# Kernel optimization log

Measured on AMD Instinct MI355X. Metric: run time of the kernel, lower is better.

## Reference

```python
import jax, jax.numpy as jnp
import numpy as np

EMBED_DIM = 1024
PROJ_DIM = 64
B, S = 8, 2048


def setup_inputs() -> dict:
    key = jax.random.key(0)
    k1, k2, k3 = jax.random.split(key, 3)
    context = jax.random.normal(k1, (S, B, EMBED_DIM), dtype=jnp.float32)
    prior = jax.random.uniform(k2, (B, S), dtype=jnp.float32)
    # xavier_uniform for (2*proj_dim, embed_dim)
    bound = float(np.sqrt(6.0 / (2 * PROJ_DIM + EMBED_DIM)))
    proj_weight = jax.random.uniform(k3, (2 * PROJ_DIM, EMBED_DIM), dtype=jnp.float32,
                                     minval=-bound, maxval=bound)
    proj_bias = jnp.zeros((2 * PROJ_DIM,), dtype=jnp.float32)
    return {"context": context, "prior": prior,
            "proj_weight": proj_weight, "proj_bias": proj_bias}


def reference(context, prior, proj_weight, proj_bias):
    # context: (S, B, E) -> (B, S, E)
    x = jnp.transpose(context, (1, 0, 2))
    b, s, e = x.shape
    qk = jnp.einsum('bse,pe->bsp', x, proj_weight) + proj_bias  # (B,S,2P)
    query, key = jnp.split(qk, 2, axis=2)
    # neighbor scores, scaled by embed_dim (as in the original)
    fwd = jnp.sum(query[:, :-1] * key[:, 1:], axis=-1) / e   # (B,S-1) score i<->i+1
    bwd = jnp.sum(query[:, 1:] * key[:, :-1], axis=-1) / e   # (B,S-1) score i<->i-1
    ninf = jnp.full((b, 1), -jnp.inf, dtype=x.dtype)
    score = jnp.stack([jnp.concatenate([fwd, ninf], axis=1),
                       jnp.concatenate([ninf, bwd], axis=1)], axis=-1)  # (B,S,2)
    prob = jax.nn.softmax(score, axis=-1)
    # torch .roll(shifts=-1) with no dims flattens the whole tensor: reproduce that
    shift_prob = jnp.roll(prob[:, :, 1].reshape(-1), -1).reshape(b, s)
    prob0 = jnp.sqrt(prob[:, :, 0] * shift_prob + 1e-6)      # (B,S)
    neighbor_attn = prior + (1.0 - prior) * prob0
    log_prob = jnp.log(neighbor_attn)
    # Original places log_prob[:, :-1] on the superdiagonal and hits it with
    # triu matmuls on both sides: C[i,j] = sum_{m=i}^{j-1} log_prob[m] for j>i.
    # Equivalent O(n^2): prefix sums cs[t] = sum_{m<t} log_prob[m].
    cs = jnp.concatenate([jnp.zeros((b, 1), dtype=x.dtype),
                          jnp.cumsum(log_prob[:, :-1], axis=1)], axis=1)  # (B,S)
    D = cs[:, None, :] - cs[:, :, None]            # D[b,i,j] = cs[j]-cs[i]
    i_idx = jnp.arange(s)
    upper = i_idx[None, :] > i_idx[:, None]        # (S,S) j>i
    M = jnp.where(upper[None], D, -D)              # C + C^T (symmetric)
    constituent_attn = jnp.exp(M)
    diag = i_idx[None, :] == i_idx[:, None]
    constituent_attn = jnp.where(diag[None], jnp.zeros((), x.dtype), constituent_attn)
    return constituent_attn, neighbor_attn
```

## Files before the change

### kernel.cpp

```cpp
#include <hip/hip_runtime.h>
#include <cstdint>
#include <cstddef>

#define E_DIM 1024
#define PD 64
#define NP 128
#define B_DIM 8
#define S_DIM 2048
#define M_TOT (B_DIM * S_DIM)

#define BMR 32
#define BK 32
#define NCHH 16

typedef __attribute__((ext_vector_type(8))) short short8v;
typedef __attribute__((ext_vector_type(4))) float f32x4;

__device__ __forceinline__ void gload16(const void* g, void* l) {
    __builtin_amdgcn_global_load_lds(
        (const __attribute__((address_space(1))) unsigned int*)g,
        (__attribute__((address_space(3))) unsigned int*)(uintptr_t)l,
        16, 0, 0);
}

__device__ __forceinline__ void cvt_hilo(const f32x4 v0, const f32x4 v1,
                                         short8v& h, short8v& l) {
    const unsigned MSK = 0xFFFF0000u;
    unsigned a0 = __float_as_uint(v0.x), a1 = __float_as_uint(v0.y);
    unsigned a2 = __float_as_uint(v0.z), a3 = __float_as_uint(v0.w);
    unsigned a4 = __float_as_uint(v1.x), a5 = __float_as_uint(v1.y);
    unsigned a6 = __float_as_uint(v1.z), a7 = __float_as_uint(v1.w);
    float l0 = v0.x - __uint_as_float(a0 & MSK);
    float l1 = v0.y - __uint_as_float(a1 & MSK);
    float l2 = v0.z - __uint_as_float(a2 & MSK);
    float l3 = v0.w - __uint_as_float(a3 & MSK);
    float l4 = v1.x - __uint_as_float(a4 & MSK);
    float l5 = v1.y - __uint_as_float(a5 & MSK);
    float l6 = v1.z - __uint_as_float(a6 & MSK);
    float l7 = v1.w - __uint_as_float(a7 & MSK);
    union { unsigned u[4]; short8v s; } H, L;
    H.u[0] = (a1 & MSK) | (a0 >> 16);
    H.u[1] = (a3 & MSK) | (a2 >> 16);
    H.u[2] = (a5 & MSK) | (a4 >> 16);
    H.u[3] = (a7 & MSK) | (a6 >> 16);
    L.u[0] = (__float_as_uint(l1) & MSK) | (__float_as_uint(l0) >> 16);
    L.u[1] = (__float_as_uint(l3) & MSK) | (__float_as_uint(l2) >> 16);
    L.u[2] = (__float_as_uint(l5) & MSK) | (__float_as_uint(l4) >> 16);
    L.u[3] = (__float_as_uint(l7) & MSK) | (__float_as_uint(l6) >> 16);
    h = H.s; l = L.s;
}

__global__ __launch_bounds__(256) void conv_w(const float* __restrict__ W,
                                              ushort* __restrict__ hiImg,
                                              ushort* __restrict__ loImg) {
    const int t = blockIdx.x * 256 + threadIdx.x;
    const int c  = t & 127;
    const int q  = (t >> 7) & 3;
    const int ch = t >> 9;
    const float* src = W + (size_t)c * E_DIM + ch * 32 + q * 8;
    const f32x4 v0 = *(const f32x4*)src;
    const f32x4 v1 = *(const f32x4*)(src + 4);
    short8v h, l;
    cvt_hilo(v0, v1, h, l);
    const size_t off = ((size_t)(ch * 4 + q) * NP + c) * 8;
    *(short8v*)&hiImg[off] = h;
    *(short8v*)&loImg[off] = l;
}

__global__ __launch_bounds__(512, 4) void gemm_qk(const float* __restrict__ A,
                                                  const ushort* __restrict__ hiImg,
                                                  const ushort* __restrict__ loImg,
                                                  const float* __restrict__ bias,
                                                  float* __restrict__ qk) {
    __shared__ __align__(16) float As[2][2][BMR][BK];
    __shared__ __align__(16) float Cred[BMR][NP];
    const int tid = threadIdx.x;
    const int m0  = blockIdx.x * BMR;
    const int w   = tid >> 6;
    const int h   = w >> 2;
    const int wv  = w & 3;
    const int ln  = tid & 63;
    const int lr  = ln >> 3;
    const int g8  = ln & 7;
    const int row16 = ln & 15;
    const int kq    = ln >> 4;
    const int r7    = row16 & 7;
    const int sg0 = ((((kq << 1) | 0) ^ r7) & 7) << 2;
    const int sg1 = ((((kq << 1) | 1) ^ r7) & 7) << 2;

    const int srow = wv * 8 + lr;
    const float* aS = A + (size_t)(m0 + srow) * E_DIM + h * (NCHH * BK)
                        + ((g8 ^ (srow & 7)) << 2);
    const ushort* hS = hiImg + (size_t)(h * NCHH) * 4096
                             + ((size_t)kq * NP + wv * 32 + row16) * 8;
    const ushort* lS = loImg + (size_t)(h * NCHH) * 4096
                             + ((size_t)kq * NP + wv * 32 + row16) * 8;

    float bias2[2];
    bias2[0] = bias[wv * 32 + row16];
    bias2[1] = bias[wv * 32 + 16 + row16];

    f32x4 acc[2][2];
#pragma unroll
    for (int i = 0; i < 2; ++i)
#pragma unroll
        for (int j = 0; j < 2; ++j) acc[i][j] = (f32x4){0.f, 0.f, 0.f, 0.f};

    short8v whA0, whA1, wlA0, wlA1;
    short8v whB0, whB1, wlB0, wlB1;

    gload16(aS, &As[h][0][wv * 8][0]);
    whA0 = *(const short8v*)(hS);
    whA1 = *(const short8v*)(hS + 128);
    wlA0 = *(const short8v*)(lS);
    wlA1 = *(const short8v*)(lS + 128);

#define GBODY(CH, WH0, WH1, WL0, WL1, NWH0, NWH1, NWL0, NWL1)                       \
    {                                                                               \
        const int buf = (CH) & 1;                                                   \
        __syncthreads();                    \
        if ((CH) + 1 < NCHH) {                                                      \
            gload16(aS + ((CH) + 1) * BK, &As[h][buf ^ 1][wv * 8][0]);              \
            NWH0 = *(const short8v*)(hS + (size_t)((CH) + 1) * 4096);               \
            NWH1 = *(const short8v*)(hS + (size_t)((CH) + 1) * 4096 + 128);         \
            NWL0 = *(const short8v*)(lS + (size_t)((CH) + 1) * 4096);               \
            NWL1 = *(const short8v*)(lS + (size_t)((CH) + 1) * 4096 + 128);         \
        }                                                                           \
        short8v ah0, al0, ah1, al1;                                                 \
        {                                                                           \
            const float* b0 = &As[h][buf][row16][0];                                \
            cvt_hilo(*(const f32x4*)(b0 + sg0), *(const f32x4*)(b0 + sg1), ah0, al0); \
            const float* b1 = &As[h][buf][16 + row16][0];                           \
            cvt_hilo(*(const f32x4*)(b1 + sg0), *(const f32x4*)(b1 + sg1), ah1, al1); \
        }                                                                           \
        acc[0][0] = __builtin_amdgcn_mfma_f32_16x16x32_bf16(ah0, WH0, acc[0][0], 0, 0, 0); \
        acc[0][0] = __builtin_amdgcn_mfma_f32_16x16x32_bf16(ah0, WL0, acc[0][0], 0, 0, 0); \
        acc[0][0] = __builtin_amdgcn_mfma_f32_16x16x32_bf16(al0, WH0, acc[0][0], 0, 0, 0); \
        acc[0][1] = __builtin_amdgcn_mfma_f32_16x16x32_bf16(ah0, WH1, acc[0][1], 0, 0, 0); \
        acc[0][1] = __builtin_amdgcn_mfma_f32_16x16x32_bf16(ah0, WL1, acc[0][1], 0, 0, 0); \
        acc[0][1] = __builtin_amdgcn_mfma_f32_16x16x32_bf16(al0, WH1, acc[0][1], 0, 0, 0); \
        acc[1][0] = __builtin_amdgcn_mfma_f32_16x16x32_bf16(ah1, WH0, acc[1][0], 0, 0, 0); \
        acc[1][0] = __builtin_amdgcn_mfma_f32_16x16x32_bf16(ah1, WL0, acc[1][0], 0, 0, 0); \
        acc[1][0] = __builtin_amdgcn_mfma_f32_16x16x32_bf16(al1, WH0, acc[1][0], 0, 0, 0); \
        acc[1][1] = __builtin_amdgcn_mfma_f32_16x16x32_bf16(ah1, WH1, acc[1][1], 0, 0, 0); \
        acc[1][1] = __builtin_amdgcn_mfma_f32_16x16x32_bf16(ah1, WL1, acc[1][1], 0, 0, 0); \
        acc[1][1] = __builtin_amdgcn_mfma_f32_16x16x32_bf16(al1, WH1, acc[1][1], 0, 0, 0); \
    }

#pragma unroll 1
    for (int c2 = 0; c2 < NCHH / 2; ++c2) {
        GBODY(2 * c2,     whA0, whA1, wlA0, wlA1, whB0, whB1, wlB0, wlB1)
        GBODY(2 * c2 + 1, whB0, whB1, wlB0, wlB1, whA0, whA1, wlA0, wlA1)
    }
#undef GBODY

    if (h == 1) {
#pragma unroll
        for (int fi = 0; fi < 2; ++fi)
#pragma unroll
            for (int fj = 0; fj < 2; ++fj)
#pragma unroll
                for (int r = 0; r < 4; ++r)
                    Cred[fi * 16 + kq * 4 + r][wv * 32 + fj * 16 + row16] = acc[fi][fj][r];
    }
    __syncthreads();
    if (h == 0) {
#pragma unroll
        for (int fi = 0; fi < 2; ++fi)
#pragma unroll
            for (int fj = 0; fj < 2; ++fj) {
#pragma unroll
                for (int r = 0; r < 4; ++r) {
                    const int mr = fi * 16 + kq * 4 + r;
                    const int p  = wv * 32 + fj * 16 + row16;
                    qk[(size_t)(m0 + mr) * NP + p] =
                        acc[fi][fj][r] + Cred[mr][p] + bias2[fj];
                }
            }
    }
}

__global__ __launch_bounds__(256) void neighbor_probs(const float* __restrict__ qk,
                                                      float* __restrict__ p0,
                                                      float* __restrict__ p1) {
    const int m = blockIdx.x * 4 + (threadIdx.x >> 6);
    const int lane = threadIdx.x & 63;
    const int s = m >> 3;
    const int b = m & 7;

    const float q = qk[(size_t)m * NP + lane];
    const float kn = (s < S_DIM - 1) ? qk[(size_t)(m + B_DIM) * NP + PD + lane] : 0.f;
    const float kp = (s > 0) ? qk[(size_t)(m - B_DIM) * NP + PD + lane] : 0.f;
    float f = q * kn;
    float g = q * kp;
#pragma unroll
    for (int off = 32; off; off >>= 1) {
        f += __shfl_xor(f, off);
        g += __shfl_xor(g, off);
    }
    if (lane == 0) {
        const float s0 = f * (1.f / (float)E_DIM);
        const float s1 = g * (1.f / (float)E_DIM);
        float P0, P1;
        if (s == S_DIM - 1) { P0 = 0.f; P1 = 1.f; }
        else if (s == 0)    { P0 = 1.f; P1 = 0.f; }
        else {
            const float mx = fmaxf(s0, s1);
            const float e0 = __expf(s0 - mx), e1 = __expf(s1 - mx);
            const float inv = 1.f / (e0 + e1);
            P0 = e0 * inv; P1 = e1 * inv;
        }
        p0[b * S_DIM + s] = P0;
        p1[b * S_DIM + s] = P1;
    }
}

__global__ __launch_bounds__(256) void combine_scan(const float* __restrict__ p0,
                                                    const float* __restrict__ p1,
                                                    const float* __restrict__ prior,
                                                    float* __restrict__ out_na,
                                                    float* __restrict__ cs) {
    const int b = blockIdx.x;
    const int tid = threadIdx.x;
    __shared__ float sh[256];

    const int base = b * S_DIM + tid * 8;
    float incl[8];
    float run = 0.f;
#pragma unroll
    for (int u = 0; u < 8; ++u) {
        const int fidx = base + u;
        int nf = fidx + 1;
        if (nf == B_DIM * S_DIM) nf = 0;
        const float P0 = p0[fidx];
        const float sp = p1[nf];
        const float pr = prior[fidx];
        const float na = pr + (1.f - pr) * sqrtf(P0 * sp + 1e-6f);
        out_na[fidx] = na;
        run += __logf(na);
        incl[u] = run;
    }
    sh[tid] = run;
    __syncthreads();
    for (int off = 1; off < 256; off <<= 1) {
        float v = sh[tid];
        if (tid >= off) v += sh[tid - off];
        __syncthreads();
        sh[tid] = v;
        __syncthreads();
    }
    const float offset = (tid > 0) ? sh[tid - 1] : 0.f;
#pragma unroll
    for (int u = 0; u < 8; ++u) {
        cs[base + u] = offset + ((u > 0) ? incl[u - 1] : 0.f);
    }
}

__global__ __launch_bounds__(256) void big_out(const float* __restrict__ cs,
                                               float* __restrict__ out) {
    const int bi = blockIdx.x;
    const int b = bi >> 11;
    const int i = bi & (S_DIM - 1);
    const float ci = cs[b * S_DIM + i];
    const float* crow = cs + (size_t)b * S_DIM;
    float* orow = out + (size_t)bi * S_DIM;
    const int j0 = threadIdx.x * 8;
#pragma unroll
    for (int h = 0; h < 2; ++h) {
        const int j = j0 + h * 4;
        const f32x4 cj = *(const f32x4*)&crow[j];
        f32x4 o;
        {
            const int jj = j + 0; const float m = (jj > i) ? (cj.x - ci) : (ci - cj.x);
            o.x = (jj == i) ? 0.f : __expf(m);
        }
        {
            const int jj = j + 1; const float m = (jj > i) ? (cj.y - ci) : (ci - cj.y);
            o.y = (jj == i) ? 0.f : __expf(m);
        }
        {
            const int jj = j + 2; const float m = (jj > i) ? (cj.z - ci) : (ci - cj.z);
            o.z = (jj == i) ? 0.f : __expf(m);
        }
        {
            const int jj = j + 3; const float m = (jj > i) ? (cj.w - ci) : (ci - cj.w);
            o.w = (jj == i) ? 0.f : __expf(m);
        }
        *(f32x4*)&orow[j] = o;
    }
}

extern "C" void kernel_launch(void* const* d_in, const int* in_sizes, int n_in,
                              void* d_out, int out_size, void* d_ws, size_t ws_size,
                              hipStream_t stream) {
    const float* context = (const float*)d_in[0];
    const float* prior   = (const float*)d_in[1];
    const float* W       = (const float*)d_in[2];
    const float* bias    = (const float*)d_in[3];
    float* out = (float*)d_out;

    float* qk = (float*)d_ws;
    float* p0 = qk + (size_t)M_TOT * NP;
    float* p1 = p0 + M_TOT;
    float* cs = p1 + M_TOT;
    ushort* hiImg = (ushort*)out;
    ushort* loImg = hiImg + (size_t)NP * E_DIM;
    float* na_out = out + (size_t)B_DIM * S_DIM * S_DIM;

    conv_w<<<64, 256, 0, stream>>>(W, hiImg, loImg);
    gemm_qk<<<M_TOT / BMR, 512, 0, stream>>>(context, hiImg, loImg, bias, qk);
    neighbor_probs<<<M_TOT / 4, 256, 0, stream>>>(qk, p0, p1);
    combine_scan<<<B_DIM, 256, 0, stream>>>(p0, p1, prior, na_out, cs);
    big_out<<<M_TOT, 256, 0, stream>>>(cs, out);
}
```

Baseline: 64.04 us.

## Fuse neighbor-score softmax into the projection GEMM with halo rows

The QK projection GEMM now computes the neighbor dot products and the 2-way softmax in its epilogue. It drops the intermediate qk buffer and the separate neighbor_probs kernel. Each block loads 48 context rows, its 32 rows plus an 8-row halo on each side, so neighbor keys are available in shared memory. The split-K across two wave halves is replaced by 4 waves that each walk the full K. This redundantly recomputes the halo rows, adding 50% more GEMM work, and gives fewer waves per block in exchange for removing a global round trip and a launch.

```diff
diff --git a/kernel.cpp b/kernel.cpp
--- a/kernel.cpp
+++ b/kernel.cpp
@@ -9,9 +9,8 @@
 #define S_DIM 2048
 #define M_TOT (B_DIM * S_DIM)
 
-#define BMR 32
 #define BK 32
-#define NCHH 16
+#define NCH (E_DIM / BK)
 
 typedef __attribute__((ext_vector_type(8))) short short8v;
 typedef __attribute__((ext_vector_type(4))) float f32x4;
@@ -50,6 +49,8 @@
     h = H.s; l = L.s;
 }
 
+#define MFMA(d, a, b) d = __builtin_amdgcn_mfma_f32_16x16x32_bf16(a, b, d, 0, 0, 0)
+
 __global__ __launch_bounds__(256) void conv_w(const float* __restrict__ W,
                                               ushort* __restrict__ hiImg,
                                               ushort* __restrict__ loImg) {
@@ -67,18 +68,18 @@
     *(short8v*)&loImg[off] = l;
 }
 
-__global__ __launch_bounds__(512, 4) void gemm_qk(const float* __restrict__ A,
-                                                  const ushort* __restrict__ hiImg,
-                                                  const ushort* __restrict__ loImg,
-                                                  const float* __restrict__ bias,
-                                                  float* __restrict__ qk) {
-    __shared__ __align__(16) float As[2][2][BMR][BK];
-    __shared__ __align__(16) float Cred[BMR][NP];
+__global__ __launch_bounds__(256, 2) void gemm_scores(const float* __restrict__ A,
+                                                      const ushort* __restrict__ hiImg,
+                                                      const ushort* __restrict__ loImg,
+                                                      const float* __restrict__ bias,
+                                                      float* __restrict__ p0,
+                                                      float* __restrict__ p1) {
+    __shared__ __align__(16) float As[2][48][BK];
+    __shared__ __align__(16) float Cmat[48][132];
     const int tid = threadIdx.x;
-    const int m0  = blockIdx.x * BMR;
+    const int g   = blockIdx.x;
+    const int m0  = g * 32;
     const int w   = tid >> 6;
-    const int h   = w >> 2;
-    const int wv  = w & 3;
     const int ln  = tid & 63;
     const int lr  = ln >> 3;
     const int g8  = ln & 7;
@@ -88,130 +89,109 @@
     const int sg0 = ((((kq << 1) | 0) ^ r7) & 7) << 2;
     const int sg1 = ((((kq << 1) | 1) ^ r7) & 7) << 2;
 
-    const int srow = wv * 8 + lr;
-    const float* aS = A + (size_t)(m0 + srow) * E_DIM + h * (NCHH * BK)
-                        + ((g8 ^ (srow & 7)) << 2);
-    const ushort* hS = hiImg + (size_t)(h * NCHH) * 4096
-                             + ((size_t)kq * NP + wv * 32 + row16) * 8;
-    const ushort* lS = loImg + (size_t)(h * NCHH) * 4096
-                             + ((size_t)kq * NP + wv * 32 + row16) * 8;
-
+    long gr1 = (long)m0 - 8 + w * 8 + lr;
+    gr1 = gr1 < 0 ? 0 : (gr1 >= M_TOT ? M_TOT - 1 : gr1);
+    const float* aP1 = A + (size_t)gr1 * E_DIM + ((g8 ^ lr) << 2);
+    const float* aP2 = aP1;
+    if (w < 2) {
+        long gr2 = (long)m0 - 8 + 32 + w * 8 + lr;
+        gr2 = gr2 < 0 ? 0 : (gr2 >= M_TOT ? M_TOT - 1 : gr2);
+        aP2 = A + (size_t)gr2 * E_DIM + ((g8 ^ lr) << 2);
+    }
+    const ushort* hS = hiImg + ((size_t)kq * NP + w * 32 + row16) * 8;
+    const ushort* lS = loImg + ((size_t)kq * NP + w * 32 + row16) * 8;
     float bias2[2];
-    bias2[0] = bias[wv * 32 + row16];
-    bias2[1] = bias[wv * 32 + 16 + row16];
-
-    f32x4 acc[2][2];
-#pragma unroll
-    for (int i = 0; i < 2; ++i)
+    bias2[0] = bias[w * 32 + row16];
+    bias2[1] = bias[w * 32 + 16 + row16];
+
+    f32x4 acc[3][2];
+#pragma unroll
+    for (int i = 0; i < 3; ++i)
 #pragma unroll
         for (int j = 0; j < 2; ++j) acc[i][j] = (f32x4){0.f, 0.f, 0.f, 0.f};
 
-    short8v whA0, whA1, wlA0, wlA1;
-    short8v whB0, whB1, wlB0, wlB1;
-
-    gload16(aS, &As[h][0][wv * 8][0]);
+    short8v whA0, whA1, wlA0, wlA1, whB0, whB1, wlB0, wlB1;
+
+    gload16(aP1, &As[0][w * 8][0]);
+    if (w < 2) gload16(aP2, &As[0][32 + w * 8][0]);
     whA0 = *(const short8v*)(hS);
     whA1 = *(const short8v*)(hS + 128);
     wlA0 = *(const short8v*)(lS);
     wlA1 = *(const short8v*)(lS + 128);
 
-#define GBODY(CH, WH0, WH1, WL0, WL1, NWH0, NWH1, NWL0, NWL1)                       \
+#define GB(CH, WH0, WH1, WL0, WL1, NWH0, NWH1, NWL0, NWL1)                          \
     {                                                                               \
         const int buf = (CH) & 1;                                                   \
-        __syncthreads();                    \
-        if ((CH) + 1 < NCHH) {                                                      \
-            gload16(aS + ((CH) + 1) * BK, &As[h][buf ^ 1][wv * 8][0]);              \
+        __syncthreads();                                                            \
+        if ((CH) + 1 < NCH) {                                                       \
+            gload16(aP1 + ((CH) + 1) * BK, &As[buf ^ 1][w * 8][0]);                 \
+            if (w < 2) gload16(aP2 + ((CH) + 1) * BK, &As[buf ^ 1][32 + w * 8][0]); \
             NWH0 = *(const short8v*)(hS + (size_t)((CH) + 1) * 4096);               \
             NWH1 = *(const short8v*)(hS + (size_t)((CH) + 1) * 4096 + 128);         \
             NWL0 = *(const short8v*)(lS + (size_t)((CH) + 1) * 4096);               \
             NWL1 = *(const short8v*)(lS + (size_t)((CH) + 1) * 4096 + 128);         \
         }                                                                           \
-        short8v ah0, al0, ah1, al1;                                                 \
-        {                                                                           \
-            const float* b0 = &As[h][buf][row16][0];                                \
-            cvt_hilo(*(const f32x4*)(b0 + sg0), *(const f32x4*)(b0 + sg1), ah0, al0); \
-            const float* b1 = &As[h][buf][16 + row16][0];                           \
-            cvt_hilo(*(const f32x4*)(b1 + sg0), *(const f32x4*)(b1 + sg1), ah1, al1); \
+        short8v ah, al;                                                             \
+        _Pragma("unroll")                                                           \
+        for (int rf = 0; rf < 3; ++rf) {                                            \
+            const float* bp = &As[buf][rf * 16 + row16][0];                         \
+            cvt_hilo(*(const f32x4*)(bp + sg0), *(const f32x4*)(bp + sg1), ah, al); \
+            MFMA(acc[rf][0], ah, WH0);                                              \
+            MFMA(acc[rf][0], ah, WL0);                                              \
+            MFMA(acc[rf][0], al, WH0);                                              \
+            MFMA(acc[rf][1], ah, WH1);                                              \
+            MFMA(acc[rf][1], ah, WL1);                                              \
+            MFMA(acc[rf][1], al, WH1);                                              \
         }                                                                           \
-        acc[0][0] = __builtin_amdgcn_mfma_f32_16x16x32_bf16(ah0, WH0, acc[0][0], 0, 0, 0); \
-        acc[0][0] = __builtin_amdgcn_mfma_f32_16x16x32_bf16(ah0, WL0, acc[0][0], 0, 0, 0); \
-        acc[0][0] = __builtin_amdgcn_mfma_f32_16x16x32_bf16(al0, WH0, acc[0][0], 0, 0, 0); \
-        acc[0][1] = __builtin_amdgcn_mfma_f32_16x16x32_bf16(ah0, WH1, acc[0][1], 0, 0, 0); \
-        acc[0][1] = __builtin_amdgcn_mfma_f32_16x16x32_bf16(ah0, WL1, acc[0][1], 0, 0, 0); \
-        acc[0][1] = __builtin_amdgcn_mfma_f32_16x16x32_bf16(al0, WH1, acc[0][1], 0, 0, 0); \
-        acc[1][0] = __builtin_amdgcn_mfma_f32_16x16x32_bf16(ah1, WH0, acc[1][0], 0, 0, 0); \
-        acc[1][0] = __builtin_amdgcn_mfma_f32_16x16x32_bf16(ah1, WL0, acc[1][0], 0, 0, 0); \
-        acc[1][0] = __builtin_amdgcn_mfma_f32_16x16x32_bf16(al1, WH0, acc[1][0], 0, 0, 0); \
-        acc[1][1] = __builtin_amdgcn_mfma_f32_16x16x32_bf16(ah1, WH1, acc[1][1], 0, 0, 0); \
-        acc[1][1] = __builtin_amdgcn_mfma_f32_16x16x32_bf16(ah1, WL1, acc[1][1], 0, 0, 0); \
-        acc[1][1] = __builtin_amdgcn_mfma_f32_16x16x32_bf16(al1, WH1, acc[1][1], 0, 0, 0); \
     }
 
 #pragma unroll 1
-    for (int c2 = 0; c2 < NCHH / 2; ++c2) {
-        GBODY(2 * c2,     whA0, whA1, wlA0, wlA1, whB0, whB1, wlB0, wlB1)
-        GBODY(2 * c2 + 1, whB0, whB1, wlB0, wlB1, whA0, whA1, wlA0, wlA1)
-    }
-#undef GBODY
-
-    if (h == 1) {
-#pragma unroll
-        for (int fi = 0; fi < 2; ++fi)
-#pragma unroll
-            for (int fj = 0; fj < 2; ++fj)
-#pragma unroll
-                for (int r = 0; r < 4; ++r)
-                    Cred[fi * 16 + kq * 4 + r][wv * 32 + fj * 16 + row16] = acc[fi][fj][r];
-    }
+    for (int c2 = 0; c2 < NCH / 2; ++c2) {
+        GB(2 * c2,     whA0, whA1, wlA0, wlA1, whB0, whB1, wlB0, wlB1)
+        GB(2 * c2 + 1, whB0, whB1, wlB0, wlB1, whA0, whA1, wlA0, wlA1)
+    }
+#undef GB
+
     __syncthreads();
-    if (h == 0) {
-#pragma unroll
-        for (int fi = 0; fi < 2; ++fi)
-#pragma unroll
-            for (int fj = 0; fj < 2; ++fj) {
-#pragma unroll
-                for (int r = 0; r < 4; ++r) {
-                    const int mr = fi * 16 + kq * 4 + r;
-                    const int p  = wv * 32 + fj * 16 + row16;
-                    qk[(size_t)(m0 + mr) * NP + p] =
-                        acc[fi][fj][r] + Cred[mr][p] + bias2[fj];
-                }
+#pragma unroll
+    for (int rf = 0; rf < 3; ++rf)
+#pragma unroll
+        for (int fj = 0; fj < 2; ++fj)
+#pragma unroll
+            for (int r = 0; r < 4; ++r)
+                Cmat[rf * 16 + kq * 4 + r][w * 32 + fj * 16 + row16] =
+                    acc[rf][fj][r] + bias2[fj];
+    __syncthreads();
+
+#pragma unroll 1
+    for (int u = 0; u < 8; ++u) {
+        const int tr = 8 + w * 8 + u;
+        const float q  = Cmat[tr][ln];
+        const float kf = Cmat[tr + 8][64 + ln];
+        const float kb = Cmat[tr - 8][64 + ln];
+        float f  = q * kf;
+        float g2 = q * kb;
+#pragma unroll
+        for (int off = 32; off; off >>= 1) {
+            f  += __shfl_xor(f, off);
+            g2 += __shfl_xor(g2, off);
+        }
+        if (ln == 0) {
+            const int s_abs = g * 4 + w;
+            float P0, P1;
+            if (s_abs == 0)              { P0 = 1.f; P1 = 0.f; }
+            else if (s_abs == S_DIM - 1) { P0 = 0.f; P1 = 1.f; }
+            else {
+                const float s0 = f  * (1.f / (float)E_DIM);
+                const float s1 = g2 * (1.f / (float)E_DIM);
+                const float mx = fmaxf(s0, s1);
+                const float e0 = __expf(s0 - mx), e1 = __expf(s1 - mx);
+                const float inv = 1.f / (e0 + e1);
+                P0 = e0 * inv; P1 = e1 * inv;
             }
-    }
-}
-
-__global__ __launch_bounds__(256) void neighbor_probs(const float* __restrict__ qk,
-                                                      float* __restrict__ p0,
-                                                      float* __restrict__ p1) {
-    const int m = blockIdx.x * 4 + (threadIdx.x >> 6);
-    const int lane = threadIdx.x & 63;
-    const int s = m >> 3;
-    const int b = m & 7;
-
-    const float q = qk[(size_t)m * NP + lane];
-    const float kn = (s < S_DIM - 1) ? qk[(size_t)(m + B_DIM) * NP + PD + lane] : 0.f;
-    const float kp = (s > 0) ? qk[(size_t)(m - B_DIM) * NP + PD + lane] : 0.f;
-    float f = q * kn;
-    float g = q * kp;
-#pragma unroll
-    for (int off = 32; off; off >>= 1) {
-        f += __shfl_xor(f, off);
-        g += __shfl_xor(g, off);
-    }
-    if (lane == 0) {
-        const float s0 = f * (1.f / (float)E_DIM);
-        const float s1 = g * (1.f / (float)E_DIM);
-        float P0, P1;
-        if (s == S_DIM - 1) { P0 = 0.f; P1 = 1.f; }
-        else if (s == 0)    { P0 = 1.f; P1 = 0.f; }
-        else {
-            const float mx = fmaxf(s0, s1);
-            const float e0 = __expf(s0 - mx), e1 = __expf(s1 - mx);
-            const float inv = 1.f / (e0 + e1);
-            P0 = e0 * inv; P1 = e1 * inv;
-        }
-        p0[b * S_DIM + s] = P0;
-        p1[b * S_DIM + s] = P1;
+            p0[u * S_DIM + s_abs] = P0;
+            p1[u * S_DIM + s_abs] = P1;
+        }
     }
 }
 
@@ -299,8 +279,7 @@
     const float* bias    = (const float*)d_in[3];
     float* out = (float*)d_out;
 
-    float* qk = (float*)d_ws;
-    float* p0 = qk + (size_t)M_TOT * NP;
+    float* p0 = (float*)d_ws;
     float* p1 = p0 + M_TOT;
     float* cs = p1 + M_TOT;
     ushort* hiImg = (ushort*)out;
@@ -308,8 +287,7 @@
     float* na_out = out + (size_t)B_DIM * S_DIM * S_DIM;
 
     conv_w<<<64, 256, 0, stream>>>(W, hiImg, loImg);
-    gemm_qk<<<M_TOT / BMR, 512, 0, stream>>>(context, hiImg, loImg, bias, qk);
-    neighbor_probs<<<M_TOT / 4, 256, 0, stream>>>(qk, p0, p1);
+    gemm_scores<<<M_TOT / 32, 256, 0, stream>>>(context, hiImg, loImg, bias, p0, p1);
     combine_scan<<<B_DIM, 256, 0, stream>>>(p0, p1, prior, na_out, cs);
     big_out<<<M_TOT, 256, 0, stream>>>(cs, out);
 }
```

After: 69.50 us. +8.5%, slower.
